# Kernel optimization log

Hardware: AMD Instinct MI355X
Metric: run time of the kernel (lower is better)

The kernel has to match this reference:

```python
import jax, jax.numpy as jnp
import numpy as np

TAU = 0.07
EPS = 1e-12  # F.normalize clamp_min eps
LAYERS = [5, 11, 17, 23]


def _l2n(x):
    # F.normalize(x, dim=-1): x / max(||x||_2, eps)
    return x / jnp.clip(jnp.linalg.norm(x, axis=-1, keepdims=True), EPS)


def _head(cls_tok, patch_tok, w_cls, w_seg, out_h, out_w):
    # cosine-similarity logits
    logits_cls = (_l2n(cls_tok) @ _l2n(w_cls).T) / TAU                      # [B,2]
    logits_seg = jnp.einsum('bnd,cd->bnc', _l2n(patch_tok), _l2n(w_seg)) / TAU  # [B,N,2]
    probs = jax.nn.softmax(logits_seg, axis=-1)                             # [B,N,2]
    B, N, _ = probs.shape
    side = int(np.sqrt(N))
    probs = probs.reshape(B, side, side, 2).transpose(0, 3, 1, 2)           # [B,2,s,s]
    # torch bilinear align_corners=False == jax half-pixel bilinear (upsampling)
    probs = jax.image.resize(probs, (B, 2, out_h, out_w), method='bilinear')
    return logits_cls, probs


def setup_inputs() -> dict:
    key = jax.random.key(0)
    B, N, D, H = 32, 1024, 1024, 512
    ks = jax.random.split(key, 4 * len(LAYERS))
    inp = {}
    for i, l in enumerate(LAYERS):
        inp[f'cls_{l}'] = jax.random.normal(ks[4 * i], (B, D), jnp.float32)
        inp[f'patch_{l}'] = jax.random.normal(ks[4 * i + 1], (B, N, D), jnp.float32)
        inp[f'w_cls_{l}'] = jax.random.normal(ks[4 * i + 2], (2, D), jnp.float32) * 0.02
        inp[f'w_seg_{l}'] = jax.random.normal(ks[4 * i + 3], (2, D), jnp.float32) * 0.02
    inp['out_h'] = H
    inp['out_w'] = H
    return inp


def reference(cls_5, patch_5, w_cls_5, w_seg_5,
              cls_11, patch_11, w_cls_11, w_seg_11,
              cls_17, patch_17, w_cls_17, w_seg_17,
              cls_23, patch_23, w_cls_23, w_seg_23,
              out_h, out_w):
    groups = [(cls_5, patch_5, w_cls_5, w_seg_5),
              (cls_11, patch_11, w_cls_11, w_seg_11),
              (cls_17, patch_17, w_cls_17, w_seg_17),
              (cls_23, patch_23, w_cls_23, w_seg_23)]
    cls_logits, seg_probs = [], []
    for (c, p, wc, ws) in groups:
        lc, sp = _head(c, p, wc, ws, out_h, out_w)
        cls_logits.append(lc)
        seg_probs.append(sp)
    # stacked over layers: [L,B,2] and [L,B,2,H,W]
    return jnp.stack(cls_logits), jnp.stack(seg_probs)
```

## Files before the change

### kernel.cpp

```cpp
#include <hip/hip_runtime.h>
#include <math.h>

#define D 1024
#define B 32
#define N 1024
#define SIDE 32
#define OUT 512
#define NLAYER 4
#define TAU_INV (1.0f/0.07f)
#define EPS_NORM 1e-12f

typedef float f32x4 __attribute__((ext_vector_type(4)));

__device__ __forceinline__ float wave_sum(float s) {
#pragma unroll
    for (int m = 32; m; m >>= 1) s += __shfl_xor(s, m);
    return s;
}

__global__ void cls_prep_kernel(const float* c0, const float* wc0,
                                const float* c1, const float* wc1,
                                const float* c2, const float* wc2,
                                const float* c3, const float* wc3,
                                const float* s0, const float* s1,
                                const float* s2, const float* s3,
                                float* out, float* what) {
    if (blockIdx.x == 32) {
        int l = threadIdx.x >> 6;
        int lane = threadIdx.x & 63;
        const float* w = (l == 0) ? s0 : (l == 1) ? s1 : (l == 2) ? s2 : s3;
        float4 wa[4], wb[4];
        float q00 = 0.f, q11 = 0.f;
#pragma unroll
        for (int kk = 0; kk < 4; ++kk) {
            int off = kk * 256 + lane * 4;
            wa[kk] = *reinterpret_cast<const float4*>(w + off);
            wb[kk] = *reinterpret_cast<const float4*>(w + D + off);
            q00 += wa[kk].x * wa[kk].x + wa[kk].y * wa[kk].y + wa[kk].z * wa[kk].z + wa[kk].w * wa[kk].w;
            q11 += wb[kk].x * wb[kk].x + wb[kk].y * wb[kk].y + wb[kk].z * wb[kk].z + wb[kk].w * wb[kk].w;
        }
        q00 = wave_sum(q00); q11 = wave_sum(q11);
        float iw0 = TAU_INV / fmaxf(sqrtf(q00), EPS_NORM);
        float iw1 = TAU_INV / fmaxf(sqrtf(q11), EPS_NORM);
        float* o = what + (size_t)l * D;
#pragma unroll
        for (int kk = 0; kk < 4; ++kk) {
            int off = kk * 256 + lane * 4;
            float4 r;
            r.x = wa[kk].x * iw0 - wb[kk].x * iw1;
            r.y = wa[kk].y * iw0 - wb[kk].y * iw1;
            r.z = wa[kk].z * iw0 - wb[kk].z * iw1;
            r.w = wa[kk].w * iw0 - wb[kk].w * iw1;
            *reinterpret_cast<float4*>(o + off) = r;
        }
        return;
    }

    int wid = blockIdx.x * 4 + (threadIdx.x >> 6);
    int lane = threadIdx.x & 63;
    int l = wid >> 5;
    int b = wid & 31;
    const float* cls; const float* wc;
    if      (l == 0) { cls = c0; wc = wc0; }
    else if (l == 1) { cls = c1; wc = wc1; }
    else if (l == 2) { cls = c2; wc = wc2; }
    else             { cls = c3; wc = wc3; }
    const float* x = cls + (size_t)b * D;

    float sxx = 0.f, sx0 = 0.f, sx1 = 0.f, q00 = 0.f, q11 = 0.f;
#pragma unroll
    for (int kk = 0; kk < 4; ++kk) {
        int off = kk * 256 + lane * 4;
        const float4 v  = *reinterpret_cast<const float4*>(x + off);
        const float4 a  = *reinterpret_cast<const float4*>(wc + off);
        const float4 bb = *reinterpret_cast<const float4*>(wc + D + off);
        sxx += v.x * v.x + v.y * v.y + v.z * v.z + v.w * v.w;
        sx0 += v.x * a.x + v.y * a.y + v.z * a.z + v.w * a.w;
        sx1 += v.x * bb.x + v.y * bb.y + v.z * bb.z + v.w * bb.w;
        q00 += a.x * a.x + a.y * a.y + a.z * a.z + a.w * a.w;
        q11 += bb.x * bb.x + bb.y * bb.y + bb.z * bb.z + bb.w * bb.w;
    }
    sxx = wave_sum(sxx); sx0 = wave_sum(sx0); sx1 = wave_sum(sx1);
    q00 = wave_sum(q00); q11 = wave_sum(q11);
    if (lane == 0) {
        float invx = 1.0f / fmaxf(sqrtf(sxx), EPS_NORM);
        float iw0  = 1.0f / fmaxf(sqrtf(q00), EPS_NORM);
        float iw1  = 1.0f / fmaxf(sqrtf(q11), EPS_NORM);
        out[((size_t)l * B + b) * 2 + 0] = sx0 * invx * iw0 * TAU_INV;
        out[((size_t)l * B + b) * 2 + 1] = sx1 * invx * iw1 * TAU_INV;
    }
}

__global__ __launch_bounds__(256) void seg_kernel(
        const float* p0, const float* p1, const float* p2, const float* p3,
        const float* what, float* probs) {
    __shared__ float wsm[D];

    int bid  = blockIdx.x;
    int base = bid * 16;
    int l    = base >> 15;
    int rem  = base & 32767;
    const float* patch = (l == 0) ? p0 : (l == 1) ? p1 : (l == 2) ? p2 : p3;

    int tid = threadIdx.x;
    *reinterpret_cast<float4*>(wsm + tid * 4) =
        *reinterpret_cast<const float4*>(what + (size_t)l * D + tid * 4);
    __syncthreads();

    int k = tid & 15;
    int r = tid >> 4;
    const float* x  = patch + (size_t)(rem + r) * D + k * 4;
    const float* wp = wsm + k * 4;

    float sxx = 0.f, sd = 0.f;
#pragma unroll
    for (int i = 0; i < 16; ++i) {
        const f32x4 v = __builtin_nontemporal_load(
            reinterpret_cast<const f32x4*>(x + i * 64));
        const float4 w = *reinterpret_cast<const float4*>(wp + i * 64);
        sxx += v.x * v.x + v.y * v.y + v.z * v.z + v.w * v.w;
        sd  += v.x * w.x + v.y * w.y + v.z * w.z + v.w * w.w;
    }
#pragma unroll
    for (int m = 1; m < 16; m <<= 1) {
        sxx += __shfl_xor(sxx, m);
        sd  += __shfl_xor(sd, m);
    }
    float diff = sd / fmaxf(sqrtf(sxx), EPS_NORM);
    float e    = __expf(-diff);
    float pr0  = 1.0f / (1.0f + e);
    float pr1  = pr0 * e;

    int lane = tid & 63;
    float a0 = __shfl(pr0, 0),  a1 = __shfl(pr0, 16);
    float a2 = __shfl(pr0, 32), a3 = __shfl(pr0, 48);
    float b0 = __shfl(pr1, 0),  b1 = __shfl(pr1, 16);
    float b2 = __shfl(pr1, 32), b3 = __shfl(pr1, 48);
    if (lane == 0) {
        int wv  = tid >> 6;
        int big = rem >> 10;
        int n0  = (rem & 1023) + wv * 4;
        float* o = probs + ((size_t)(l * B + big) * 2) * N;
        *reinterpret_cast<float4*>(o + n0)     = make_float4(a0, a1, a2, a3);
        *reinterpret_cast<float4*>(o + N + n0) = make_float4(b0, b1, b2, b3);
    }
}

__global__ __launch_bounds__(256) void upsample_kernel(const float* probs, float* out) {
    __shared__ float rowbuf[64 * 32];

    int img   = blockIdx.x >> 3;
    int chunk = blockIdx.x & 7;
    const float* S = probs + (size_t)img * (SIDE * SIDE);

    for (int e = threadIdx.x; e < 64 * 32; e += 256) {
        int r = e >> 5;
        int xs = e & 31;
        int gy = chunk * 64 + r;
        float fy = fmaxf(((float)gy + 0.5f) * 0.0625f - 0.5f, 0.0f);
        int y0 = min((int)fy, SIDE - 1);
        int y1 = min(y0 + 1, SIDE - 1);
        float wy = fy - (float)y0;
        float a = S[y0 * SIDE + xs];
        float b = S[y1 * SIDE + xs];
        rowbuf[e] = a + wy * (b - a);
    }
    __syncthreads();

    int tid = threadIdx.x;
    int xv  = tid & 127;
    int rhalf = tid >> 7;
    float fx0 = fmaxf(((float)(4 * xv) + 0.5f) * 0.0625f - 0.5f, 0.0f);
    int x0 = min((int)fx0, SIDE - 1);
    int x1 = min(x0 + 1, SIDE - 1);
    float wx[4];
#pragma unroll
    for (int j = 0; j < 4; ++j) {
        float fx = fmaxf(((float)(4 * xv + j) + 0.5f) * 0.0625f - 0.5f, 0.0f);
        wx[j] = fx - (float)x0;
    }

    float4* obase = reinterpret_cast<float4*>(out) + (size_t)img * (OUT * OUT / 4);
#pragma unroll 8
    for (int it = 0; it < 32; ++it) {
        int r = it * 2 + rhalf;
        const float* rb = rowbuf + r * 32;
        float r0 = rb[x0];
        float d  = rb[x1] - r0;
        float4 o;
        o.x = r0 + wx[0] * d;
        o.y = r0 + wx[1] * d;
        o.z = r0 + wx[2] * d;
        o.w = r0 + wx[3] * d;
        int gy = chunk * 64 + r;
        obase[(size_t)gy * (OUT / 4) + xv] = o;
    }
}

extern "C" void kernel_launch(void* const* d_in, const int* in_sizes, int n_in,
                              void* d_out, int out_size, void* d_ws, size_t ws_size,
                              hipStream_t stream) {
    const float* cls[4];  const float* patch[4];
    const float* wcls[4]; const float* wseg[4];
    for (int l = 0; l < 4; ++l) {
        cls[l]   = (const float*)d_in[4 * l + 0];
        patch[l] = (const float*)d_in[4 * l + 1];
        wcls[l]  = (const float*)d_in[4 * l + 2];
        wseg[l]  = (const float*)d_in[4 * l + 3];
    }
    float* out = (float*)d_out;
    float* seg_out = out + NLAYER * B * 2;

    float* ws_what  = (float*)d_ws;
    float* ws_probs = ws_what + NLAYER * D;

    cls_prep_kernel<<<33, 256, 0, stream>>>(cls[0], wcls[0], cls[1], wcls[1],
                                            cls[2], wcls[2], cls[3], wcls[3],
                                            wseg[0], wseg[1], wseg[2], wseg[3],
                                            out, ws_what);

    seg_kernel<<<8192, 256, 0, stream>>>(patch[0], patch[1], patch[2], patch[3],
                                         ws_what, ws_probs);

    upsample_kernel<<<2048, 256, 0, stream>>>(ws_probs, seg_out);
}
```

Before: 138.0 us.

## Software-pipeline seg and upsample across layers in fused interleaved launches

Replaces the separate seg and upsample kernels with one dual-role kernel launched five times. Each launch does the seg dot-product pass for layer l while its interleaved blocks upsample layer l-1's probabilities, so the read-heavy patch stream and the write-heavy output stream overlap. The cost is more launches and per-launch tail effects. Stream ordering between launches keeps the dependency between the two stages correct.

```diff
diff --git a/kernel.cpp b/kernel.cpp
--- a/kernel.cpp
+++ b/kernel.cpp
@@ -91,109 +91,114 @@
     }
 }
 
-__global__ __launch_bounds__(256) void seg_kernel(
-        const float* p0, const float* p1, const float* p2, const float* p3,
-        const float* what, float* probs) {
-    __shared__ float wsm[D];
-
-    int bid  = blockIdx.x;
-    int base = bid * 16;
-    int l    = base >> 15;
-    int rem  = base & 32767;
-    const float* patch = (l == 0) ? p0 : (l == 1) ? p1 : (l == 2) ? p2 : p3;
+__global__ __launch_bounds__(256) void pipe_kernel(
+        const float* patch, const float* what, float* probs, float* up_out,
+        int seg_layer, int nseg, int up_layer) {
+    __shared__ float smem[2048];
+
+    int seg_id = -1, up_id = -1;
+    if (nseg > 0 && up_layer >= 0) {
+        int grp = blockIdx.x / 5, sub = blockIdx.x - grp * 5;
+        if (sub == 4) up_id = grp; else seg_id = grp * 4 + sub;
+    } else if (nseg > 0) {
+        seg_id = blockIdx.x;
+    } else {
+        up_id = blockIdx.x;
+    }
 
     int tid = threadIdx.x;
-    *reinterpret_cast<float4*>(wsm + tid * 4) =
-        *reinterpret_cast<const float4*>(what + (size_t)l * D + tid * 4);
-    __syncthreads();
-
-    int k = tid & 15;
-    int r = tid >> 4;
-    const float* x  = patch + (size_t)(rem + r) * D + k * 4;
-    const float* wp = wsm + k * 4;
-
-    float sxx = 0.f, sd = 0.f;
-#pragma unroll
-    for (int i = 0; i < 16; ++i) {
-        const f32x4 v = __builtin_nontemporal_load(
-            reinterpret_cast<const f32x4*>(x + i * 64));
-        const float4 w = *reinterpret_cast<const float4*>(wp + i * 64);
-        sxx += v.x * v.x + v.y * v.y + v.z * v.z + v.w * v.w;
-        sd  += v.x * w.x + v.y * w.y + v.z * w.z + v.w * w.w;
-    }
-#pragma unroll
-    for (int m = 1; m < 16; m <<= 1) {
-        sxx += __shfl_xor(sxx, m);
-        sd  += __shfl_xor(sd, m);
-    }
-    float diff = sd / fmaxf(sqrtf(sxx), EPS_NORM);
-    float e    = __expf(-diff);
-    float pr0  = 1.0f / (1.0f + e);
-    float pr1  = pr0 * e;
-
-    int lane = tid & 63;
-    float a0 = __shfl(pr0, 0),  a1 = __shfl(pr0, 16);
-    float a2 = __shfl(pr0, 32), a3 = __shfl(pr0, 48);
-    float b0 = __shfl(pr1, 0),  b1 = __shfl(pr1, 16);
-    float b2 = __shfl(pr1, 32), b3 = __shfl(pr1, 48);
-    if (lane == 0) {
-        int wv  = tid >> 6;
-        int big = rem >> 10;
-        int n0  = (rem & 1023) + wv * 4;
-        float* o = probs + ((size_t)(l * B + big) * 2) * N;
-        *reinterpret_cast<float4*>(o + n0)     = make_float4(a0, a1, a2, a3);
-        *reinterpret_cast<float4*>(o + N + n0) = make_float4(b0, b1, b2, b3);
-    }
-}
-
-__global__ __launch_bounds__(256) void upsample_kernel(const float* probs, float* out) {
-    __shared__ float rowbuf[64 * 32];
-
-    int img   = blockIdx.x >> 3;
-    int chunk = blockIdx.x & 7;
-    const float* S = probs + (size_t)img * (SIDE * SIDE);
-
-    for (int e = threadIdx.x; e < 64 * 32; e += 256) {
-        int r = e >> 5;
-        int xs = e & 31;
-        int gy = chunk * 64 + r;
-        float fy = fmaxf(((float)gy + 0.5f) * 0.0625f - 0.5f, 0.0f);
-        int y0 = min((int)fy, SIDE - 1);
-        int y1 = min(y0 + 1, SIDE - 1);
-        float wy = fy - (float)y0;
-        float a = S[y0 * SIDE + xs];
-        float b = S[y1 * SIDE + xs];
-        rowbuf[e] = a + wy * (b - a);
-    }
-    __syncthreads();
-
-    int tid = threadIdx.x;
-    int xv  = tid & 127;
-    int rhalf = tid >> 7;
-    float fx0 = fmaxf(((float)(4 * xv) + 0.5f) * 0.0625f - 0.5f, 0.0f);
-    int x0 = min((int)fx0, SIDE - 1);
-    int x1 = min(x0 + 1, SIDE - 1);
-    float wx[4];
-#pragma unroll
-    for (int j = 0; j < 4; ++j) {
-        float fx = fmaxf(((float)(4 * xv + j) + 0.5f) * 0.0625f - 0.5f, 0.0f);
-        wx[j] = fx - (float)x0;
-    }
-
-    float4* obase = reinterpret_cast<float4*>(out) + (size_t)img * (OUT * OUT / 4);
+
+    if (seg_id >= 0) {
+        float* wsm = smem;
+        int rem = seg_id * 16;
+        *reinterpret_cast<float4*>(wsm + tid * 4) =
+            *reinterpret_cast<const float4*>(what + (size_t)seg_layer * D + tid * 4);
+        __syncthreads();
+
+        int k = tid & 15;
+        int r = tid >> 4;
+        const float* x  = patch + (size_t)(rem + r) * D + k * 4;
+        const float* wp = wsm + k * 4;
+
+        float sxx = 0.f, sd = 0.f;
+#pragma unroll
+        for (int i = 0; i < 16; ++i) {
+            const f32x4 v = __builtin_nontemporal_load(
+                reinterpret_cast<const f32x4*>(x + i * 64));
+            const float4 w = *reinterpret_cast<const float4*>(wp + i * 64);
+            sxx += v.x * v.x + v.y * v.y + v.z * v.z + v.w * v.w;
+            sd  += v.x * w.x + v.y * w.y + v.z * w.z + v.w * w.w;
+        }
+#pragma unroll
+        for (int m = 1; m < 16; m <<= 1) {
+            sxx += __shfl_xor(sxx, m);
+            sd  += __shfl_xor(sd, m);
+        }
+        float diff = sd / fmaxf(sqrtf(sxx), EPS_NORM);
+        float e    = __expf(-diff);
+        float pr0  = 1.0f / (1.0f + e);
+        float pr1  = pr0 * e;
+
+        int lane = tid & 63;
+        float a0 = __shfl(pr0, 0),  a1 = __shfl(pr0, 16);
+        float a2 = __shfl(pr0, 32), a3 = __shfl(pr0, 48);
+        float b0 = __shfl(pr1, 0),  b1 = __shfl(pr1, 16);
+        float b2 = __shfl(pr1, 32), b3 = __shfl(pr1, 48);
+        if (lane == 0) {
+            int wv  = tid >> 6;
+            int big = rem >> 10;
+            int n0  = (rem & 1023) + wv * 4;
+            float* o = probs + ((size_t)(seg_layer * B + big) * 2) * N;
+            *reinterpret_cast<float4*>(o + n0)     = make_float4(a0, a1, a2, a3);
+            *reinterpret_cast<float4*>(o + N + n0) = make_float4(b0, b1, b2, b3);
+        }
+    } else {
+        float* rowbuf = smem;
+        int plane = up_layer * (B * 2) + (up_id >> 3);
+        int chunk = up_id & 7;
+        const float* S = probs + (size_t)plane * (SIDE * SIDE);
+
+        for (int e = tid; e < 64 * 32; e += 256) {
+            int r = e >> 5;
+            int xs = e & 31;
+            int gy = chunk * 64 + r;
+            float fy = fmaxf(((float)gy + 0.5f) * 0.0625f - 0.5f, 0.0f);
+            int y0 = min((int)fy, SIDE - 1);
+            int y1 = min(y0 + 1, SIDE - 1);
+            float wy = fy - (float)y0;
+            float a = S[y0 * SIDE + xs];
+            float b = S[y1 * SIDE + xs];
+            rowbuf[e] = a + wy * (b - a);
+        }
+        __syncthreads();
+
+        int xv  = tid & 127;
+        int rhalf = tid >> 7;
+        float fx0 = fmaxf(((float)(4 * xv) + 0.5f) * 0.0625f - 0.5f, 0.0f);
+        int x0 = min((int)fx0, SIDE - 1);
+        int x1 = min(x0 + 1, SIDE - 1);
+        float wx[4];
+#pragma unroll
+        for (int j = 0; j < 4; ++j) {
+            float fx = fmaxf(((float)(4 * xv + j) + 0.5f) * 0.0625f - 0.5f, 0.0f);
+            wx[j] = fx - (float)x0;
+        }
+
+        float4* obase = reinterpret_cast<float4*>(up_out) + (size_t)plane * (OUT * OUT / 4);
 #pragma unroll 8
-    for (int it = 0; it < 32; ++it) {
-        int r = it * 2 + rhalf;
-        const float* rb = rowbuf + r * 32;
-        float r0 = rb[x0];
-        float d  = rb[x1] - r0;
-        float4 o;
-        o.x = r0 + wx[0] * d;
-        o.y = r0 + wx[1] * d;
-        o.z = r0 + wx[2] * d;
-        o.w = r0 + wx[3] * d;
-        int gy = chunk * 64 + r;
-        obase[(size_t)gy * (OUT / 4) + xv] = o;
+        for (int it = 0; it < 32; ++it) {
+            int r = it * 2 + rhalf;
+            const float* rb = rowbuf + r * 32;
+            float r0 = rb[x0];
+            float d  = rb[x1] - r0;
+            float4 o;
+            o.x = r0 + wx[0] * d;
+            o.y = r0 + wx[1] * d;
+            o.z = r0 + wx[2] * d;
+            o.w = r0 + wx[3] * d;
+            int gy = chunk * 64 + r;
+            obase[(size_t)gy * (OUT / 4) + xv] = o;
+        }
     }
 }
 
@@ -219,8 +224,9 @@
                                             wseg[0], wseg[1], wseg[2], wseg[3],
                                             out, ws_what);
 
-    seg_kernel<<<8192, 256, 0, stream>>>(patch[0], patch[1], patch[2], patch[3],
-                                         ws_what, ws_probs);
-
-    upsample_kernel<<<2048, 256, 0, stream>>>(ws_probs, seg_out);
-}
+    pipe_kernel<<<2048, 256, 0, stream>>>(patch[0], ws_what, ws_probs, seg_out, 0, 2048, -1);
+    pipe_kernel<<<2560, 256, 0, stream>>>(patch[1], ws_what, ws_probs, seg_out, 1, 2048, 0);
+    pipe_kernel<<<2560, 256, 0, stream>>>(patch[2], ws_what, ws_probs, seg_out, 2, 2048, 1);
+    pipe_kernel<<<2560, 256, 0, stream>>>(patch[3], ws_what, ws_probs, seg_out, 3, 2048, 2);
+    pipe_kernel<<< 512, 256, 0, stream>>>(patch[3], ws_what, ws_probs, seg_out, -1, 0, 3);
+}
```

Result: slower. 154.4 us (+11.9%).
